# Kernel optimization log

Hardware: AMD Instinct MI355X
Metric: run time of the kernel (lower is better)

Reference implementation:

```python
import jax, jax.numpy as jnp
import numpy as np

B, NK, NQ, DK, DQ, H, DV = 16, 256, 256, 256, 256, 128, 256
MASK_VAL = -1000000.0

def setup_inputs() -> dict:
    key = jax.random.key(0)
    ks = jax.random.split(key, 7)
    return {
        "key": jax.random.normal(ks[0], (B, NK, DK), dtype=jnp.float32),
        "query": jax.random.normal(ks[1], (B, NQ, DQ), dtype=jnp.float32),
        "value": jax.random.normal(ks[2], (B, NQ, DV), dtype=jnp.float32),
        "valid_lens": jax.random.randint(ks[3], (B,), 1, NQ + 1, dtype=jnp.int32),
        "Wk": jax.random.normal(ks[4], (DK, H), dtype=jnp.float32) / np.sqrt(DK),
        "Wq": jax.random.normal(ks[5], (DQ, H), dtype=jnp.float32) / np.sqrt(DQ),
        "wv": jax.random.normal(ks[6], (H,), dtype=jnp.float32) / np.sqrt(H),
    }

def reference(key, query, value, valid_lens, Wk, Wq, wv):
    k = key @ Wk                      # (B, NK, H)
    q = query @ Wq                    # (B, NQ, H)
    # note: original unsqueezes key at dim 2, query at dim 1 -> (B, NK, NQ, H)
    feature = jnp.tanh(k[:, :, None, :] + q[:, None, :, :])
    scores = jnp.einsum('bkqh,h->bkq', feature, wv)   # (B, NK, NQ)
    # mask along last (query) axis per batch, as repeat_interleave does
    pos = jnp.arange(scores.shape[-1])[None, None, :]
    masked = jnp.where(pos < valid_lens[:, None, None], scores, MASK_VAL)
    attn = jax.nn.softmax(masked, axis=-1)            # (B, NK, NQ)
    return jnp.einsum('bkq,bqd->bkd', attn, value)    # (B, NK, DV)
```

## Files before the change

### kernel.cpp

```cpp
#include <hip/hip_runtime.h>

#define B_   16
#define NK_  256
#define NQ_  256
#define DK_  256
#define H_   128
#define DV_  256

#define C2X 2.8853900817779268f
#define L2E 1.4426950408889634f
#define MASKV -1.0e5f

typedef float f4 __attribute__((ext_vector_type(4)));
typedef short s4v    __attribute__((ext_vector_type(4)));
typedef short bf16x8 __attribute__((ext_vector_type(8)));

__device__ __forceinline__ float exp2_fast(float x) { return __builtin_amdgcn_exp2f(x); }
__device__ __forceinline__ float rcp_fast(float x)  { return __builtin_amdgcn_rcpf(x); }

__device__ __forceinline__ unsigned bf16_rne(float x) {
    unsigned u = __builtin_bit_cast(unsigned, x);
    return (u + 0x7FFFu + ((u >> 16) & 1u)) >> 16;
}
__device__ __forceinline__ float bf16_to_f(unsigned h) {
    return __builtin_bit_cast(float, h << 16);
}

__global__ __launch_bounds__(256) void proj_kernel(
    const float* __restrict__ key, const float* __restrict__ query,
    const float* __restrict__ Wk,  const float* __restrict__ Wq,
    float* __restrict__ kfE, float* __restrict__ qE4)
{
    __shared__ alignas(16) short Ah_s[32 * 264];
    __shared__ alignas(16) short Al_s[32 * 264];

    const int blk = blockIdx.x;
    const int tid = threadIdx.x;
    const bool isQ = blk >= 128;
    const int mbase = (blk & 127) << 5;

    const float* __restrict__ Ag = isQ ? query : key;
    const float* __restrict__ Wg = isQ ? Wq : Wk;

    {
        const int r  = tid >> 3;
        const int kc = (tid & 7) << 5;
        const f4* src = (const f4*)(Ag + (size_t)(mbase + r) * DK_ + kc);
        s4v* dh = (s4v*)(Ah_s + r * 264 + kc);
        s4v* dl = (s4v*)(Al_s + r * 264 + kc);
#pragma unroll
        for (int i = 0; i < 8; ++i) {
            f4 v = src[i];
            s4v h, l;
#pragma unroll
            for (int c = 0; c < 4; ++c) {
                unsigned hb = bf16_rne(v[c]);
                h[c] = (short)hb;
                l[c] = (short)bf16_rne(v[c] - bf16_to_f(hb));
            }
            dh[i] = h;
            dl[i] = l;
        }
    }
    __syncthreads();

    const int w  = tid >> 6;
    const int l  = tid & 63;
    const int lg = l >> 4;
    const int ln = l & 15;

    f4 acc[2][2] = {};

#pragma unroll
    for (int ks = 0; ks < 8; ++ks) {
        const int k0 = ks << 5;

        bf16x8 bh[2], bl[2];
#pragma unroll
        for (int nt = 0; nt < 2; ++nt) {
            const float* bp = Wg + (size_t)(k0 + (lg << 3)) * H_
                              + (w << 5) + (nt << 4) + ln;
            float bv[8];
#pragma unroll
            for (int j = 0; j < 8; ++j) bv[j] = bp[(size_t)j * H_];
#pragma unroll
            for (int j = 0; j < 8; ++j) {
                unsigned hb = bf16_rne(bv[j]);
                bh[nt][j] = (short)hb;
                bl[nt][j] = (short)bf16_rne(bv[j] - bf16_to_f(hb));
            }
        }

        bf16x8 ah[2], al[2];
#pragma unroll
        for (int mt = 0; mt < 2; ++mt) {
            const int m = (mt << 4) + ln;
            ah[mt] = *(const bf16x8*)(Ah_s + m * 264 + k0 + (lg << 3));
            al[mt] = *(const bf16x8*)(Al_s + m * 264 + k0 + (lg << 3));
        }

#pragma unroll
        for (int mt = 0; mt < 2; ++mt)
#pragma unroll
            for (int nt = 0; nt < 2; ++nt) {
                acc[mt][nt] = __builtin_amdgcn_mfma_f32_16x16x32_bf16(
                    ah[mt], bh[nt], acc[mt][nt], 0, 0, 0);
                acc[mt][nt] = __builtin_amdgcn_mfma_f32_16x16x32_bf16(
                    al[mt], bh[nt], acc[mt][nt], 0, 0, 0);
                acc[mt][nt] = __builtin_amdgcn_mfma_f32_16x16x32_bf16(
                    ah[mt], bl[nt], acc[mt][nt], 0, 0, 0);
            }
    }

#pragma unroll
    for (int mt = 0; mt < 2; ++mt)
#pragma unroll
        for (int nt = 0; nt < 2; ++nt)
#pragma unroll
            for (int r = 0; r < 4; ++r) {
                const float e = exp2_fast(C2X * acc[mt][nt][r]);
                const int R = mbase + (mt << 4) + (lg << 2) + r;
                const int h = (w << 5) + (nt << 4) + ln;
                if (!isQ) {
                    kfE[(size_t)R * H_ + h] = e;
                } else {
                    const int b = R >> 8, q = R & 255;
                    qE4[(((size_t)(b * 32 + (h >> 2))) * NQ_ + q) * 4 + (h & 3)] = e;
                }
            }
}

__global__ __launch_bounds__(512, 4) void attn_kernel(
    const float* __restrict__ kfE, const float* __restrict__ qE4,
    const float* __restrict__ value, const int* __restrict__ vlens,
    const float* __restrict__ wv, float* __restrict__ out)
{
    __shared__ alignas(16) float at_s[256 * 8];
    __shared__ alignas(16) float scratch[8192];

    const int x    = blockIdx.x;
    const int g    = x >> 4;
    const int b    = ((x & 15) + ((x >> 8) << 3)) & 15;
    const int k0   = g << 3;
    const int tid  = threadIdx.x;
    const int lane = tid & 63;
    const int wu   = __builtin_amdgcn_readfirstlane(tid >> 6);
    const int valid  = vlens[b];
    const int nchunk = (valid + 63) >> 6;

    float sumwv;
    {
        f4 sw = {0.f, 0.f, 0.f, 0.f};
#pragma unroll
        for (int i = 0; i < 32; ++i) sw += ((const f4*)wv)[i];
        sumwv = (sw[0] + sw[1]) + (sw[2] + sw[3]);
    }

    float* sc_s = scratch;

    {
        const int c  = wu >> 1;
        const int rh = wu & 1;
        if (c < nchunk) {
            const float* ekb = kfE + ((size_t)(b * NK_ + k0 + rh * 4)) * H_;
            const f4*    eqp = (const f4*)qE4 + ((size_t)b << 13) + (c << 6) + lane;
            const f4*    wvf = (const f4*)wv;
            float acc[4][2];
#pragma unroll
            for (int r = 0; r < 4; ++r) { acc[r][0] = 0.f; acc[r][1] = 0.f; }
#pragma unroll 4
            for (int h4 = 0; h4 < 32; ++h4) {
                const f4 e  = eqp[h4 << 8];
                const f4 w4 = wvf[h4];
#pragma unroll
                for (int r = 0; r < 4; ++r) {
                    const f4 ek = *(const f4*)(ekb + r * H_ + (h4 << 2));
                    acc[r][0] = fmaf(w4[0], rcp_fast(fmaf(ek[0], e[0], 1.f)), acc[r][0]);
                    acc[r][1] = fmaf(w4[1], rcp_fast(fmaf(ek[1], e[1], 1.f)), acc[r][1]);
                    acc[r][0] = fmaf(w4[2], rcp_fast(fmaf(ek[2], e[2], 1.f)), acc[r][0]);
                    acc[r][1] = fmaf(w4[3], rcp_fast(fmaf(ek[3], e[3], 1.f)), acc[r][1]);
                }
            }
            const int q = (c << 6) + lane;
#pragma unroll
            for (int r = 0; r < 4; ++r)
                sc_s[(rh * 4 + r) * 260 + q] = sumwv - 2.f * (acc[r][0] + acc[r][1]);
        }
    }
    __syncthreads();

    {
        const float* row = sc_s + wu * 260;
        float s[4];
        float m = MASKV;
#pragma unroll
        for (int j = 0; j < 4; ++j) {
            const int q = (j << 6) + lane;
            s[j] = (q < valid) ? row[q] : MASKV;
            m = fmaxf(m, s[j]);
        }
#pragma unroll
        for (int off = 32; off >= 1; off >>= 1)
            m = fmaxf(m, __shfl_xor(m, off, 64));
        float ssum = 0.f;
#pragma unroll
        for (int j = 0; j < 4; ++j) {
            s[j] = exp2_fast(L2E * (s[j] - m));
            ssum += s[j];
        }
#pragma unroll
        for (int off = 32; off >= 1; off >>= 1)
            ssum += __shfl_xor(ssum, off, 64);
        const float inv = rcp_fast(ssum);
#pragma unroll
        for (int j = 0; j < 4; ++j)
            at_s[(((j << 6) + lane) << 3) + wu] = s[j] * inv;
    }
    __syncthreads();

    float* red = scratch;
    {
        const int d4 = lane << 2;
        const float* vb = value + (size_t)b * (NQ_ * DV_) + d4;
        f4 o[8];
#pragma unroll
        for (int k = 0; k < 8; ++k) o[k] = (f4){0.f, 0.f, 0.f, 0.f};
#pragma unroll 4
        for (int q = wu; q < valid; q += 8) {
            const f4 v   = *(const f4*)(vb + (size_t)q * DV_);
            const f4 alo = *(const f4*)(at_s + (q << 3));
            const f4 ahi = *(const f4*)(at_s + (q << 3) + 4);
            o[0] += alo[0] * v; o[1] += alo[1] * v;
            o[2] += alo[2] * v; o[3] += alo[3] * v;
            o[4] += ahi[0] * v; o[5] += ahi[1] * v;
            o[6] += ahi[2] * v; o[7] += ahi[3] * v;
        }
        if (wu < 4) {
            float* rp = red + (wu << 11) + d4;
#pragma unroll
            for (int k = 0; k < 8; ++k) *(f4*)(rp + (k << 8)) = o[k];
        }
        __syncthreads();
        if (wu >= 4) {
            float* rp = red + ((wu - 4) << 11) + d4;
#pragma unroll
            for (int k = 0; k < 8; ++k) {
                f4* p = (f4*)(rp + (k << 8));
                *p += o[k];
            }
        }
        __syncthreads();
        const float* rp = red + (wu << 8) + d4;
        f4 oo = *(const f4*)(rp)        + *(const f4*)(rp + 2048)
              + *(const f4*)(rp + 4096) + *(const f4*)(rp + 6144);
        *(f4*)(out + ((size_t)(b * NK_ + k0 + wu)) * DV_ + d4) = oo;
    }
}

extern "C" void kernel_launch(void* const* d_in, const int* in_sizes, int n_in,
                              void* d_out, int out_size, void* d_ws, size_t ws_size,
                              hipStream_t stream)
{
    const float* key   = (const float*)d_in[0];
    const float* query = (const float*)d_in[1];
    const float* value = (const float*)d_in[2];
    const int*   vlens = (const int*)  d_in[3];
    const float* Wk    = (const float*)d_in[4];
    const float* Wq    = (const float*)d_in[5];
    const float* wv    = (const float*)d_in[6];
    float* outp = (float*)d_out;

    float* kfE = (float*)d_ws;
    float* qE4 = kfE + (size_t)B_ * NK_ * H_;

    hipLaunchKernelGGL(proj_kernel, dim3(256), dim3(256), 0, stream,
                       key, query, Wk, Wq, kfE, qE4);
    hipLaunchKernelGGL(attn_kernel, dim3(512), dim3(512), 0, stream,
                       kfE, qE4, value, vlens, wv, outp);
}
```

Measured before the change: 101.0 us.

## Halve projection tile rows, load A directly, stage output in LDS for coalesced stores

The projection kernel now handles 16 rows per block instead of 32, so it launches twice as many blocks to spread the work over more CUs. It drops the LDS staging of the bf16 hi/lo split of A, and each lane loads and splits its own A fragment straight from global memory. The exp results are written to an LDS tile and then stored to kfE and qE4 as coalesced float4 writes, replacing scattered scalar stores. The cost is that each block reloads the W fragments for fewer rows, which doubles total W traffic, and a sync is added before the stores.

```diff
diff --git a/kernel.cpp b/kernel.cpp
--- a/kernel.cpp
+++ b/kernel.cpp
@@ -31,49 +31,41 @@
     const float* __restrict__ Wk,  const float* __restrict__ Wq,
     float* __restrict__ kfE, float* __restrict__ qE4)
 {
-    __shared__ alignas(16) short Ah_s[32 * 264];
-    __shared__ alignas(16) short Al_s[32 * 264];
+    __shared__ alignas(16) float E_s[16 * 132];
 
     const int blk = blockIdx.x;
     const int tid = threadIdx.x;
-    const bool isQ = blk >= 128;
-    const int mbase = (blk & 127) << 5;
+    const bool isQ = blk >= 256;
+    const int mbase = (blk & 255) << 4;
 
     const float* __restrict__ Ag = isQ ? query : key;
     const float* __restrict__ Wg = isQ ? Wq : Wk;
-
-    {
-        const int r  = tid >> 3;
-        const int kc = (tid & 7) << 5;
-        const f4* src = (const f4*)(Ag + (size_t)(mbase + r) * DK_ + kc);
-        s4v* dh = (s4v*)(Ah_s + r * 264 + kc);
-        s4v* dl = (s4v*)(Al_s + r * 264 + kc);
-#pragma unroll
-        for (int i = 0; i < 8; ++i) {
-            f4 v = src[i];
-            s4v h, l;
-#pragma unroll
-            for (int c = 0; c < 4; ++c) {
-                unsigned hb = bf16_rne(v[c]);
-                h[c] = (short)hb;
-                l[c] = (short)bf16_rne(v[c] - bf16_to_f(hb));
-            }
-            dh[i] = h;
-            dl[i] = l;
-        }
-    }
-    __syncthreads();
 
     const int w  = tid >> 6;
     const int l  = tid & 63;
     const int lg = l >> 4;
     const int ln = l & 15;
 
-    f4 acc[2][2] = {};
+    f4 acc[2] = {};
+
+    const float* arow = Ag + (size_t)(mbase + ln) * DK_ + (lg << 3);
 
 #pragma unroll
     for (int ks = 0; ks < 8; ++ks) {
         const int k0 = ks << 5;
+
+        bf16x8 ah, al;
+        {
+            const f4 a0 = *(const f4*)(arow + k0);
+            const f4 a1 = *(const f4*)(arow + k0 + 4);
+            float av[8] = {a0[0], a0[1], a0[2], a0[3], a1[0], a1[1], a1[2], a1[3]};
+#pragma unroll
+            for (int j = 0; j < 8; ++j) {
+                unsigned hb = bf16_rne(av[j]);
+                ah[j] = (short)hb;
+                al[j] = (short)bf16_rne(av[j] - bf16_to_f(hb));
+            }
+        }
 
         bf16x8 bh[2], bl[2];
 #pragma unroll
@@ -91,43 +83,43 @@
             }
         }
 
-        bf16x8 ah[2], al[2];
-#pragma unroll
-        for (int mt = 0; mt < 2; ++mt) {
-            const int m = (mt << 4) + ln;
-            ah[mt] = *(const bf16x8*)(Ah_s + m * 264 + k0 + (lg << 3));
-            al[mt] = *(const bf16x8*)(Al_s + m * 264 + k0 + (lg << 3));
-        }
-
-#pragma unroll
-        for (int mt = 0; mt < 2; ++mt)
-#pragma unroll
-            for (int nt = 0; nt < 2; ++nt) {
-                acc[mt][nt] = __builtin_amdgcn_mfma_f32_16x16x32_bf16(
-                    ah[mt], bh[nt], acc[mt][nt], 0, 0, 0);
-                acc[mt][nt] = __builtin_amdgcn_mfma_f32_16x16x32_bf16(
-                    al[mt], bh[nt], acc[mt][nt], 0, 0, 0);
-                acc[mt][nt] = __builtin_amdgcn_mfma_f32_16x16x32_bf16(
-                    ah[mt], bl[nt], acc[mt][nt], 0, 0, 0);
-            }
-    }
-
-#pragma unroll
-    for (int mt = 0; mt < 2; ++mt)
-#pragma unroll
-        for (int nt = 0; nt < 2; ++nt)
-#pragma unroll
-            for (int r = 0; r < 4; ++r) {
-                const float e = exp2_fast(C2X * acc[mt][nt][r]);
-                const int R = mbase + (mt << 4) + (lg << 2) + r;
-                const int h = (w << 5) + (nt << 4) + ln;
-                if (!isQ) {
-                    kfE[(size_t)R * H_ + h] = e;
-                } else {
-                    const int b = R >> 8, q = R & 255;
-                    qE4[(((size_t)(b * 32 + (h >> 2))) * NQ_ + q) * 4 + (h & 3)] = e;
-                }
-            }
+#pragma unroll
+        for (int nt = 0; nt < 2; ++nt) {
+            acc[nt] = __builtin_amdgcn_mfma_f32_16x16x32_bf16(ah, bh[nt], acc[nt], 0, 0, 0);
+            acc[nt] = __builtin_amdgcn_mfma_f32_16x16x32_bf16(al, bh[nt], acc[nt], 0, 0, 0);
+            acc[nt] = __builtin_amdgcn_mfma_f32_16x16x32_bf16(ah, bl[nt], acc[nt], 0, 0, 0);
+        }
+    }
+
+#pragma unroll
+    for (int nt = 0; nt < 2; ++nt)
+#pragma unroll
+        for (int r = 0; r < 4; ++r)
+            E_s[((lg << 2) + r) * 132 + (w << 5) + (nt << 4) + ln] =
+                exp2_fast(C2X * acc[nt][r]);
+    __syncthreads();
+
+    if (!isQ) {
+#pragma unroll
+        for (int i = 0; i < 2; ++i) {
+            const int idx = tid + (i << 8);
+            const int r   = idx >> 5;
+            const int c4  = (idx & 31) << 2;
+            *(f4*)(kfE + (size_t)(mbase + r) * H_ + c4) =
+                *(const f4*)(E_s + r * 132 + c4);
+        }
+    } else {
+        const int b  = mbase >> 8;
+        const int q0 = mbase & 255;
+        f4* dstb = (f4*)qE4 + (size_t)b * (32 * NQ_) + q0;
+#pragma unroll
+        for (int i = 0; i < 2; ++i) {
+            const int h4   = (tid >> 4) + (i << 4);
+            const int qloc = tid & 15;
+            dstb[(size_t)h4 * NQ_ + qloc] =
+                *(const f4*)(E_s + qloc * 132 + (h4 << 2));
+        }
+    }
 }
 
 __global__ __launch_bounds__(512, 4) void attn_kernel(
@@ -273,7 +265,7 @@
     float* kfE = (float*)d_ws;
     float* qE4 = kfE + (size_t)B_ * NK_ * H_;
 
-    hipLaunchKernelGGL(proj_kernel, dim3(256), dim3(256), 0, stream,
+    hipLaunchKernelGGL(proj_kernel, dim3(512), dim3(256), 0, stream,
                        key, query, Wk, Wq, kfE, qE4);
     hipLaunchKernelGGL(attn_kernel, dim3(512), dim3(512), 0, stream,
                        kfE, qE4, value, vlens, wv, outp);
```

Result: no change. 100.7 us (-0.4%).
